# Performance work log

Hardware: AMD Instinct MI355X
Metric: run time of the kernel (lower is better)

Reference implementation:

```python
import jax, jax.numpy as jnp
import numpy as np

# snntorch atan surrogate spike (alpha=2): fwd heaviside, bwd 1/(1+(pi*x)^2)
@jax.custom_vjp
def atan_spike(x):
    return (x > 0).astype(x.dtype)

def _atan_fwd(x):
    return atan_spike(x), x

def _atan_bwd(x, g):
    return (g / (1.0 + (jnp.pi * x) ** 2),)

atan_spike.defvjp(_atan_fwd, _atan_bwd)

B, C, T, H, O = 2048, 5, 2048, 16, 2

def setup_inputs() -> dict:
    key = jax.random.key(0)
    ks = jax.random.split(key, 6)
    x = jax.random.normal(ks[0], (B, C, T), dtype=jnp.float32)
    conv_w = jax.random.normal(ks[1], (H, C, 3), dtype=jnp.float32) * (1.0 / np.sqrt(C * 3))
    conv_b = jax.random.normal(ks[2], (H,), dtype=jnp.float32) * 0.01
    bn_gamma = jnp.ones((H,), jnp.float32)
    bn_beta = jnp.zeros((H,), jnp.float32)
    bn_mean = jnp.zeros((H,), jnp.float32)   # BatchNorm1d running stats (eval mode)
    bn_var = jnp.ones((H,), jnp.float32)
    fc_w = jax.random.normal(ks[3], (O, H), dtype=jnp.float32) * (1.0 / np.sqrt(H))
    fc_b = jax.random.normal(ks[4], (O,), dtype=jnp.float32) * 0.01
    beta1 = jnp.float32(0.8)   # snn.Leaky learn_beta=True -> scalar param
    beta2 = jnp.float32(0.8)
    return dict(x=x, conv_w=conv_w, conv_b=conv_b, bn_gamma=bn_gamma, bn_beta=bn_beta,
                bn_mean=bn_mean, bn_var=bn_var, fc_w=fc_w, fc_b=fc_b,
                beta1=beta1, beta2=beta2)

def reference(x, conv_w, conv_b, bn_gamma, bn_beta, bn_mean, bn_var, fc_w, fc_b, beta1, beta2):
    EPS, THR = 1e-5, 1.0
    # Conv1d(k=3, pad=1) on a length-1 signal: only the middle tap contributes.
    w_mid = conv_w[:, :, 1]                      # [H, C]
    scale = bn_gamma / jnp.sqrt(bn_var + EPS)    # fold BN affine
    b1 = jnp.clip(beta1, 0.0, 1.0)               # snntorch clamps learned beta
    b2 = jnp.clip(beta2, 0.0, 1.0)
    xT = jnp.transpose(x, (2, 0, 1))             # [T, B, C]
    dt = x.dtype
    mem1_0 = jnp.zeros((x.shape[0], w_mid.shape[0]), dt)
    mem2_0 = jnp.zeros((x.shape[0], fc_w.shape[0]), dt)
    acc_0 = jnp.zeros_like(mem2_0)

    def step(carry, xt):
        mem1, mem2, acc = carry
        feat = (xt * 2.0) @ w_mid.T + conv_b                 # conv1d -> [B, H]
        feat = (feat - bn_mean) * scale + bn_beta            # BN (running stats)
        # snntorch Leaky (reset_mechanism='subtract'): reset from PREVIOUS mem, detached
        reset1 = jax.lax.stop_gradient((mem1 > THR).astype(dt))
        mem1 = b1 * mem1 + feat - reset1 * THR
        spk1 = atan_spike(mem1 - THR)
        cur2 = spk1 @ fc_w.T + fc_b                          # [B, O]
        reset2 = jax.lax.stop_gradient((mem2 > THR).astype(dt))
        mem2 = b2 * mem2 + cur2 - reset2 * THR
        spk2 = atan_spike(mem2 - THR)
        return (mem1, mem2, acc + spk2), None

    (_, _, acc), _ = jax.lax.scan(step, (mem1_0, mem2_0, acc_0), xT)
    return acc  # sum of output spikes over time, [B, num_classes]
```

## Files before the change

### kernel.cpp

```cpp
#include <hip/hip_runtime.h>
#include <type_traits>

typedef float v2f __attribute__((ext_vector_type(2)));

#define BB 2048
#define CC 5
#define TT 2048
#define HH 16
#define OO 2

#define NCH  32
#define CHT  (TT / NCH)
#define WARM 96

__device__ __forceinline__ float comp4(const float4& v, int j) {
    return j == 0 ? v.x : (j == 1 ? v.y : (j == 2 ? v.z : v.w));
}
__device__ __forceinline__ v2f fma2(v2f a, v2f b, v2f c) {
    return __builtin_elementwise_fma(a, b, c);
}

#define HP 8

__global__ __launch_bounds__(64, 1) void snn_laneb_kernel(
    const float* __restrict__ x,
    const float* __restrict__ conv_w,
    const float* __restrict__ conv_b,
    const float* __restrict__ bn_gamma,
    const float* __restrict__ bn_beta,
    const float* __restrict__ bn_mean,
    const float* __restrict__ bn_var,
    const float* __restrict__ fc_w,
    const float* __restrict__ fc_b,
    const float* __restrict__ beta1p,
    const float* __restrict__ beta2p,
    float* __restrict__ out)
{
    const int b     = blockIdx.x * 64 + threadIdx.x;
    const int chunk = blockIdx.y;

    const float b1 = fminf(fmaxf(beta1p[0], 0.0f), 1.0f);
    const float b2 = fminf(fmaxf(beta2p[0], 0.0f), 1.0f);
    const v2f b1v = {b1, b1};

    v2f wp[CC][HP], effbp[HP], fw0p[HP], fw1p[HP];
#pragma unroll
    for (int hp = 0; hp < HP; ++hp) {
        {
            const int h = 2 * hp;
            const float sc = bn_gamma[h] * rsqrtf(bn_var[h] + 1e-5f);
#pragma unroll
            for (int c = 0; c < CC; ++c)
                wp[c][hp].x = 2.0f * conv_w[h * (CC * 3) + c * 3 + 1] * sc;
            effbp[hp].x = (conv_b[h] - bn_mean[h]) * sc + bn_beta[h];
            fw0p[hp].x = fc_w[h];
            fw1p[hp].x = fc_w[HH + h];
        }
        {
            const int h = 2 * hp + 1;
            const float sc = bn_gamma[h] * rsqrtf(bn_var[h] + 1e-5f);
#pragma unroll
            for (int c = 0; c < CC; ++c)
                wp[c][hp].y = 2.0f * conv_w[h * (CC * 3) + c * 3 + 1] * sc;
            effbp[hp].y = (conv_b[h] - bn_mean[h]) * sc + bn_beta[h];
            fw0p[hp].y = fc_w[h];
            fw1p[hp].y = fc_w[HH + h];
        }
    }
    const float fb0 = fc_b[0], fb1 = fc_b[1];

    const float* xb = x + (size_t)b * CC * TT;

    const int t_start = chunk * CHT;
    int tw            = t_start - WARM;
    if (tw < 0) tw = 0;
    const int t_end   = t_start + CHT;
    const int ngroups = (t_end - tw) >> 2;
    const int warm_g  = (t_start - tw) >> 2;

    v2f mem1p[HP] = {}, sp[HP] = {};
    float mem2_0 = 0.0f, mem2_1 = 0.0f, s2f0 = 0.0f, s2f1 = 0.0f;
    float acc0 = 0.0f, acc1 = 0.0f;

    auto ldg = [&](float4 (&buf)[CC], int t) __attribute__((always_inline)) {
#pragma unroll
        for (int c = 0; c < CC; ++c)
            buf[c] = *reinterpret_cast<const float4*>(xb + c * TT + t);
    };

    float4 bufA[CC], bufB[CC], bufC[CC], bufD[CC];
    ldg(bufA, tw);
    ldg(bufB, tw + 4);
    ldg(bufC, tw + 8);
    ldg(bufD, tw + 12);

    auto step4 = [&](const float4 (&cur)[CC], auto ACCC) __attribute__((always_inline)) {
#pragma unroll
        for (int j = 0; j < 4; ++j) {
            v2f xv[CC];
#pragma unroll
            for (int c = 0; c < CC; ++c) {
                const float xs = comp4(cur[c], j);
                xv[c].x = xs; xv[c].y = xs;
            }

            v2f r0p = {0.0f, 0.0f}, r1p = {0.0f, 0.0f};
#pragma unroll
            for (int hp = 0; hp < HP; ++hp) {
                v2f f = effbp[hp];
#pragma unroll
                for (int c = 0; c < CC; ++c)
                    f = fma2(xv[c], wp[c][hp], f);

                const v2f m = fma2(b1v, mem1p[hp], f - sp[hp]);
                mem1p[hp] = m;
                v2f s;
                s.x = m.x > 1.0f ? 1.0f : 0.0f;
                s.y = m.y > 1.0f ? 1.0f : 0.0f;
                sp[hp] = s;
                r0p = fma2(s, fw0p[hp], r0p);
                r1p = fma2(s, fw1p[hp], r1p);
            }
            const float cur2_0 = r0p.x + r0p.y + fb0;
            const float cur2_1 = r1p.x + r1p.y + fb1;

            mem2_0 = fmaf(b2, mem2_0, cur2_0 - s2f0);
            s2f0 = mem2_0 > 1.0f ? 1.0f : 0.0f;
            mem2_1 = fmaf(b2, mem2_1, cur2_1 - s2f1);
            s2f1 = mem2_1 > 1.0f ? 1.0f : 0.0f;

            if constexpr (decltype(ACCC)::value) {
                acc0 += s2f0;
                acc1 += s2f1;
            }
        }
    };

    const int nquads = ngroups >> 2;
    const int wquads = warm_g >> 2;
    const int tlast  = t_end - 4;

#define RUN_QUAD(ACCC)                                                   \
    {                                                                    \
        int t0 = tw + (4 * q + 4) * 4; if (t0 > tlast) t0 = tlast;       \
        int t1 = tw + (4 * q + 5) * 4; if (t1 > tlast) t1 = tlast;       \
        int t2 = tw + (4 * q + 6) * 4; if (t2 > tlast) t2 = tlast;       \
        int t3 = tw + (4 * q + 7) * 4; if (t3 > tlast) t3 = tlast;       \
        step4(bufA, ACCC); ldg(bufA, t0);                                \
        step4(bufB, ACCC); ldg(bufB, t1);                                \
        step4(bufC, ACCC); ldg(bufC, t2);                                \
        step4(bufD, ACCC); ldg(bufD, t3);                                \
    }

#pragma unroll 1
    for (int q = 0; q < wquads; ++q)
        RUN_QUAD((std::integral_constant<bool, false>{}));
#pragma unroll 1
    for (int q = wquads; q < nquads; ++q)
        RUN_QUAD((std::integral_constant<bool, true>{}));
#undef RUN_QUAD

    atomicAdd(&out[(size_t)b * OO + 0], acc0);
    atomicAdd(&out[(size_t)b * OO + 1], acc1);
}

extern "C" void kernel_launch(void* const* d_in, const int* in_sizes, int n_in,
                              void* d_out, int out_size, void* d_ws, size_t ws_size,
                              hipStream_t stream) {
    const float* x        = (const float*)d_in[0];
    const float* conv_w   = (const float*)d_in[1];
    const float* conv_b   = (const float*)d_in[2];
    const float* bn_gamma = (const float*)d_in[3];
    const float* bn_beta  = (const float*)d_in[4];
    const float* bn_mean  = (const float*)d_in[5];
    const float* bn_var   = (const float*)d_in[6];
    const float* fc_w     = (const float*)d_in[7];
    const float* fc_b     = (const float*)d_in[8];
    const float* beta1    = (const float*)d_in[9];
    const float* beta2    = (const float*)d_in[10];
    float* out = (float*)d_out;

    hipMemsetAsync(out, 0, (size_t)out_size * sizeof(float), stream);

    dim3 grid(BB / 64, NCH);
    dim3 block(64);
    snn_laneb_kernel<<<grid, block, 0, stream>>>(
        x, conv_w, conv_b, bn_gamma, bn_beta, bn_mean, bn_var,
        fc_w, fc_b, beta1, beta2, out);
}
```

Before: 88.33 us.

## Transpose input to time-major layout before scan for coalesced loads

Adds a shared-memory transpose kernel that rewrites x from [B,C,T] to [C,T,B] in workspace, then runs the scan kernel reading coalesced per-timestep values across batch lanes. The old layout had each lane reading float4 strided by C*T, giving poorly coalesced accesses. The change pays for an extra full read and write of the 84 MB input and a second launch, and it falls back to the old kernel when the workspace is too small.

```diff
diff --git a/kernel.cpp b/kernel.cpp
--- a/kernel.cpp
+++ b/kernel.cpp
@@ -12,6 +12,11 @@
 #define NCH  32
 #define CHT  (TT / NCH)
 #define WARM 96
+#define HP   8
+
+#define TTL 32
+#define BTL 256
+#define XT_BYTES ((size_t)CC * TT * BB * 4)
 
 __device__ __forceinline__ float comp4(const float4& v, int j) {
     return j == 0 ? v.x : (j == 1 ? v.y : (j == 2 ? v.z : v.w));
@@ -20,9 +25,177 @@
     return __builtin_elementwise_fma(a, b, c);
 }
 
-#define HP 8
-
-__global__ __launch_bounds__(64, 1) void snn_laneb_kernel(
+__global__ __launch_bounds__(256) void transpose_kernel(
+    const float* __restrict__ x, float* __restrict__ xT)
+{
+    __shared__ float tile[TTL][BTL + 1];
+    const int c   = blockIdx.z;
+    const int tb  = blockIdx.x * TTL;
+    const int bb  = blockIdx.y * BTL;
+    const int tid = threadIdx.x;
+
+    const int s  = tid & 7;
+    const int br = tid >> 3;
+#pragma unroll
+    for (int i = 0; i < 8; ++i) {
+        const int b_local = br + i * 32;
+        const float4 v = *reinterpret_cast<const float4*>(
+            x + (size_t)(bb + b_local) * (CC * TT) + (size_t)c * TT + tb + 4 * s);
+        tile[4 * s + 0][b_local] = v.x;
+        tile[4 * s + 1][b_local] = v.y;
+        tile[4 * s + 2][b_local] = v.z;
+        tile[4 * s + 3][b_local] = v.w;
+    }
+    __syncthreads();
+
+#pragma unroll
+    for (int t = 0; t < TTL; ++t)
+        xT[((size_t)c * TT + tb + t) * BB + bb + tid] = tile[t][tid];
+}
+
+__global__ __launch_bounds__(64, 1) void snn_scanT_kernel(
+    const float* __restrict__ xT,
+    const float* __restrict__ conv_w,
+    const float* __restrict__ conv_b,
+    const float* __restrict__ bn_gamma,
+    const float* __restrict__ bn_beta,
+    const float* __restrict__ bn_mean,
+    const float* __restrict__ bn_var,
+    const float* __restrict__ fc_w,
+    const float* __restrict__ fc_b,
+    const float* __restrict__ beta1p,
+    const float* __restrict__ beta2p,
+    float* __restrict__ out)
+{
+    const int b     = blockIdx.x * 64 + threadIdx.x;
+    const int chunk = blockIdx.y;
+
+    const float b1 = fminf(fmaxf(beta1p[0], 0.0f), 1.0f);
+    const float b2 = fminf(fmaxf(beta2p[0], 0.0f), 1.0f);
+    const v2f b1v = {b1, b1};
+
+    v2f wp[CC][HP], effbp[HP], fw0p[HP], fw1p[HP];
+#pragma unroll
+    for (int hp = 0; hp < HP; ++hp) {
+        {
+            const int h = 2 * hp;
+            const float sc = bn_gamma[h] * rsqrtf(bn_var[h] + 1e-5f);
+#pragma unroll
+            for (int c = 0; c < CC; ++c)
+                wp[c][hp].x = 2.0f * conv_w[h * (CC * 3) + c * 3 + 1] * sc;
+            effbp[hp].x = (conv_b[h] - bn_mean[h]) * sc + bn_beta[h];
+            fw0p[hp].x = fc_w[h];
+            fw1p[hp].x = fc_w[HH + h];
+        }
+        {
+            const int h = 2 * hp + 1;
+            const float sc = bn_gamma[h] * rsqrtf(bn_var[h] + 1e-5f);
+#pragma unroll
+            for (int c = 0; c < CC; ++c)
+                wp[c][hp].y = 2.0f * conv_w[h * (CC * 3) + c * 3 + 1] * sc;
+            effbp[hp].y = (conv_b[h] - bn_mean[h]) * sc + bn_beta[h];
+            fw0p[hp].y = fc_w[h];
+            fw1p[hp].y = fc_w[HH + h];
+        }
+    }
+    const float fb0 = fc_b[0], fb1 = fc_b[1];
+
+    const int t_start = chunk * CHT;
+    int tw            = t_start - WARM;
+    if (tw < 0) tw = 0;
+    const int t_end   = t_start + CHT;
+    const int ngroups = (t_end - tw) >> 2;
+    const int warm_g  = (t_start - tw) >> 2;
+
+    v2f mem1p[HP] = {}, sp[HP] = {};
+    float mem2_0 = 0.0f, mem2_1 = 0.0f, s2f0 = 0.0f, s2f1 = 0.0f;
+    float acc0 = 0.0f, acc1 = 0.0f;
+
+    auto ldg = [&](float (&buf)[CC][4], int t) __attribute__((always_inline)) {
+#pragma unroll
+        for (int c = 0; c < CC; ++c)
+#pragma unroll
+            for (int j = 0; j < 4; ++j)
+                buf[c][j] = xT[((size_t)c * TT + t + j) * BB + b];
+    };
+
+    float bufA[CC][4], bufB[CC][4], bufC[CC][4], bufD[CC][4];
+    ldg(bufA, tw);
+    ldg(bufB, tw + 4);
+    ldg(bufC, tw + 8);
+    ldg(bufD, tw + 12);
+
+    auto step4 = [&](const float (&cur)[CC][4], auto ACCC) __attribute__((always_inline)) {
+#pragma unroll
+        for (int j = 0; j < 4; ++j) {
+            v2f xv[CC];
+#pragma unroll
+            for (int c = 0; c < CC; ++c) {
+                const float xs = cur[c][j];
+                xv[c].x = xs; xv[c].y = xs;
+            }
+
+            v2f r0p = {0.0f, 0.0f}, r1p = {0.0f, 0.0f};
+#pragma unroll
+            for (int hp = 0; hp < HP; ++hp) {
+                v2f f = effbp[hp];
+#pragma unroll
+                for (int c = 0; c < CC; ++c)
+                    f = fma2(xv[c], wp[c][hp], f);
+
+                const v2f m = fma2(b1v, mem1p[hp], f - sp[hp]);
+                mem1p[hp] = m;
+                v2f s;
+                s.x = m.x > 1.0f ? 1.0f : 0.0f;
+                s.y = m.y > 1.0f ? 1.0f : 0.0f;
+                sp[hp] = s;
+                r0p = fma2(s, fw0p[hp], r0p);
+                r1p = fma2(s, fw1p[hp], r1p);
+            }
+            const float cur2_0 = r0p.x + r0p.y + fb0;
+            const float cur2_1 = r1p.x + r1p.y + fb1;
+
+            mem2_0 = fmaf(b2, mem2_0, cur2_0 - s2f0);
+            s2f0 = mem2_0 > 1.0f ? 1.0f : 0.0f;
+            mem2_1 = fmaf(b2, mem2_1, cur2_1 - s2f1);
+            s2f1 = mem2_1 > 1.0f ? 1.0f : 0.0f;
+
+            if constexpr (decltype(ACCC)::value) {
+                acc0 += s2f0;
+                acc1 += s2f1;
+            }
+        }
+    };
+
+    const int nquads = ngroups >> 2;
+    const int wquads = warm_g >> 2;
+    const int tlast  = t_end - 4;
+
+#define RUN_QUAD(ACCC)                                                   \
+    {                                                                    \
+        int t0 = tw + (4 * q + 4) * 4; if (t0 > tlast) t0 = tlast;       \
+        int t1 = tw + (4 * q + 5) * 4; if (t1 > tlast) t1 = tlast;       \
+        int t2 = tw + (4 * q + 6) * 4; if (t2 > tlast) t2 = tlast;       \
+        int t3 = tw + (4 * q + 7) * 4; if (t3 > tlast) t3 = tlast;       \
+        step4(bufA, ACCC); ldg(bufA, t0);                                \
+        step4(bufB, ACCC); ldg(bufB, t1);                                \
+        step4(bufC, ACCC); ldg(bufC, t2);                                \
+        step4(bufD, ACCC); ldg(bufD, t3);                                \
+    }
+
+#pragma unroll 1
+    for (int q = 0; q < wquads; ++q)
+        RUN_QUAD((std::integral_constant<bool, false>{}));
+#pragma unroll 1
+    for (int q = wquads; q < nquads; ++q)
+        RUN_QUAD((std::integral_constant<bool, true>{}));
+#undef RUN_QUAD
+
+    atomicAdd(&out[(size_t)b * OO + 0], acc0);
+    atomicAdd(&out[(size_t)b * OO + 1], acc1);
+}
+
+__global__ __launch_bounds__(64, 1) void snn_laneb_fb_kernel(
     const float* __restrict__ x,
     const float* __restrict__ conv_w,
     const float* __restrict__ conv_b,
@@ -103,7 +276,6 @@
                 const float xs = comp4(cur[c], j);
                 xv[c].x = xs; xv[c].y = xs;
             }
-
             v2f r0p = {0.0f, 0.0f}, r1p = {0.0f, 0.0f};
 #pragma unroll
             for (int hp = 0; hp < HP; ++hp) {
@@ -111,7 +283,6 @@
 #pragma unroll
                 for (int c = 0; c < CC; ++c)
                     f = fma2(xv[c], wp[c][hp], f);
-
                 const v2f m = fma2(b1v, mem1p[hp], f - sp[hp]);
                 mem1p[hp] = m;
                 v2f s;
@@ -123,12 +294,10 @@
             }
             const float cur2_0 = r0p.x + r0p.y + fb0;
             const float cur2_1 = r1p.x + r1p.y + fb1;
-
             mem2_0 = fmaf(b2, mem2_0, cur2_0 - s2f0);
             s2f0 = mem2_0 > 1.0f ? 1.0f : 0.0f;
             mem2_1 = fmaf(b2, mem2_1, cur2_1 - s2f1);
             s2f1 = mem2_1 > 1.0f ? 1.0f : 0.0f;
-
             if constexpr (decltype(ACCC)::value) {
                 acc0 += s2f0;
                 acc1 += s2f1;
@@ -182,9 +351,18 @@
 
     hipMemsetAsync(out, 0, (size_t)out_size * sizeof(float), stream);
 
-    dim3 grid(BB / 64, NCH);
-    dim3 block(64);
-    snn_laneb_kernel<<<grid, block, 0, stream>>>(
-        x, conv_w, conv_b, bn_gamma, bn_beta, bn_mean, bn_var,
-        fc_w, fc_b, beta1, beta2, out);
-}
+    if (ws_size >= XT_BYTES) {
+        float* xT = (float*)d_ws;
+        dim3 tgrid(TT / TTL, BB / BTL, CC);
+        transpose_kernel<<<tgrid, 256, 0, stream>>>(x, xT);
+        dim3 grid(BB / 64, NCH);
+        snn_scanT_kernel<<<grid, dim3(64), 0, stream>>>(
+            xT, conv_w, conv_b, bn_gamma, bn_beta, bn_mean, bn_var,
+            fc_w, fc_b, beta1, beta2, out);
+    } else {
+        dim3 grid(BB / 64, NCH);
+        snn_laneb_fb_kernel<<<grid, dim3(64), 0, stream>>>(
+            x, conv_w, conv_b, bn_gamma, bn_beta, bn_mean, bn_var,
+            fc_w, fc_b, beta1, beta2, out);
+    }
+}
```

Result: slower. 93.84 us (+6.2%).

## Split hidden units across lane pairs and stage coalesced input tiles through LDS

Applied to the files above, without the earlier changes.

Each batch row is now handled by two lanes, each owning 8 of the 16 hidden units, and the two partial fc sums are combined with a DPP swap. Input is loaded cooperatively in coalesced float4 chunks into a double-buffered LDS tile instead of per-lane strided global loads. The grid doubles to give more waves and a shorter per-lane dependency chain. In exchange it adds LDS traffic, cross-lane DPP ops and duplicated layer-2 work on both lanes of a pair.

```diff
diff --git a/kernel.cpp b/kernel.cpp
--- a/kernel.cpp
+++ b/kernel.cpp
@@ -19,10 +19,12 @@
 __device__ __forceinline__ v2f fma2(v2f a, v2f b, v2f c) {
     return __builtin_elementwise_fma(a, b, c);
 }
-
-#define HP 8
-
-__global__ __launch_bounds__(64, 1) void snn_laneb_kernel(
+__device__ __forceinline__ float qswap_add(float v) {
+    int s = __builtin_amdgcn_update_dpp(0, __float_as_int(v), 0xB1, 0xf, 0xf, true);
+    return v + __int_as_float(s);
+}
+
+__global__ __launch_bounds__(64) void snn_fused_kernel(
     const float* __restrict__ x,
     const float* __restrict__ conv_w,
     const float* __restrict__ conv_b,
@@ -36,18 +38,26 @@
     const float* __restrict__ beta2p,
     float* __restrict__ out)
 {
-    const int b     = blockIdx.x * 64 + threadIdx.x;
+    __shared__ float4 lds[2][CC][4][32];
+
+    const int lane  = threadIdx.x;
+    const int b0    = blockIdx.x * 32;
+    const int bown  = lane >> 1;
+    const int hb    = (lane & 1) * 8;
     const int chunk = blockIdx.y;
+
+    const int sbc  = lane >> 2;
+    const int st4  = lane & 3;
 
     const float b1 = fminf(fmaxf(beta1p[0], 0.0f), 1.0f);
     const float b2 = fminf(fmaxf(beta2p[0], 0.0f), 1.0f);
     const v2f b1v = {b1, b1};
 
-    v2f wp[CC][HP], effbp[HP], fw0p[HP], fw1p[HP];
-#pragma unroll
-    for (int hp = 0; hp < HP; ++hp) {
+    v2f wp[CC][4], effbp[4], fw0p[4], fw1p[4];
+#pragma unroll
+    for (int hp = 0; hp < 4; ++hp) {
         {
-            const int h = 2 * hp;
+            const int h = hb + 2 * hp;
             const float sc = bn_gamma[h] * rsqrtf(bn_var[h] + 1e-5f);
 #pragma unroll
             for (int c = 0; c < CC; ++c)
@@ -57,7 +67,7 @@
             fw1p[hp].x = fc_w[HH + h];
         }
         {
-            const int h = 2 * hp + 1;
+            const int h = hb + 2 * hp + 1;
             const float sc = bn_gamma[h] * rsqrtf(bn_var[h] + 1e-5f);
 #pragma unroll
             for (int c = 0; c < CC; ++c)
@@ -69,30 +79,40 @@
     }
     const float fb0 = fc_b[0], fb1 = fc_b[1];
 
-    const float* xb = x + (size_t)b * CC * TT;
-
     const int t_start = chunk * CHT;
     int tw            = t_start - WARM;
     if (tw < 0) tw = 0;
     const int t_end   = t_start + CHT;
-    const int ngroups = (t_end - tw) >> 2;
-    const int warm_g  = (t_start - tw) >> 2;
-
-    v2f mem1p[HP] = {}, sp[HP] = {};
+    const int S       = (t_end - tw) >> 4;
+    const int warmS   = (t_start - tw) >> 4;
+
+    v2f mem1p[4] = {}, sp[4] = {};
     float mem2_0 = 0.0f, mem2_1 = 0.0f, s2f0 = 0.0f, s2f1 = 0.0f;
     float acc0 = 0.0f, acc1 = 0.0f;
 
-    auto ldg = [&](float4 (&buf)[CC], int t) __attribute__((always_inline)) {
-#pragma unroll
-        for (int c = 0; c < CC; ++c)
-            buf[c] = *reinterpret_cast<const float4*>(xb + c * TT + t);
-    };
-
-    float4 bufA[CC], bufB[CC], bufC[CC], bufD[CC];
-    ldg(bufA, tw);
-    ldg(bufB, tw + 4);
-    ldg(bufC, tw + 8);
-    ldg(bufD, tw + 12);
+    float4 st[10];
+
+#define STAGE_LOAD(TSB)                                                      \
+    {                                                                        \
+        _Pragma("unroll")                                                    \
+        for (int i = 0; i < 10; ++i) {                                       \
+            const int bc = i * 16 + sbc;                                     \
+            const int bs = bc & 31, cs = bc >> 5;                            \
+            st[i] = *reinterpret_cast<const float4*>(                        \
+                x + (size_t)(b0 + bs) * (CC * TT) + (size_t)cs * TT +        \
+                (TSB) + st4 * 4);                                            \
+        }                                                                    \
+    }
+
+#define STAGE_WRITE(BUF)                                                     \
+    {                                                                        \
+        _Pragma("unroll")                                                    \
+        for (int i = 0; i < 10; ++i) {                                       \
+            const int bc = i * 16 + sbc;                                     \
+            const int bs = bc & 31, cs = bc >> 5;                            \
+            lds[BUF][cs][st4][bs] = st[i];                                   \
+        }                                                                    \
+    }
 
     auto step4 = [&](const float4 (&cur)[CC], auto ACCC) __attribute__((always_inline)) {
 #pragma unroll
@@ -106,7 +126,7 @@
 
             v2f r0p = {0.0f, 0.0f}, r1p = {0.0f, 0.0f};
 #pragma unroll
-            for (int hp = 0; hp < HP; ++hp) {
+            for (int hp = 0; hp < 4; ++hp) {
                 v2f f = effbp[hp];
 #pragma unroll
                 for (int c = 0; c < CC; ++c)
@@ -121,8 +141,8 @@
                 r0p = fma2(s, fw0p[hp], r0p);
                 r1p = fma2(s, fw1p[hp], r1p);
             }
-            const float cur2_0 = r0p.x + r0p.y + fb0;
-            const float cur2_1 = r1p.x + r1p.y + fb1;
+            const float cur2_0 = qswap_add(r0p.x + r0p.y) + fb0;
+            const float cur2_1 = qswap_add(r1p.x + r1p.y) + fb1;
 
             mem2_0 = fmaf(b2, mem2_0, cur2_0 - s2f0);
             s2f0 = mem2_0 > 1.0f ? 1.0f : 0.0f;
@@ -136,32 +156,39 @@
         }
     };
 
-    const int nquads = ngroups >> 2;
-    const int wquads = warm_g >> 2;
-    const int tlast  = t_end - 4;
-
-#define RUN_QUAD(ACCC)                                                   \
-    {                                                                    \
-        int t0 = tw + (4 * q + 4) * 4; if (t0 > tlast) t0 = tlast;       \
-        int t1 = tw + (4 * q + 5) * 4; if (t1 > tlast) t1 = tlast;       \
-        int t2 = tw + (4 * q + 6) * 4; if (t2 > tlast) t2 = tlast;       \
-        int t3 = tw + (4 * q + 7) * 4; if (t3 > tlast) t3 = tlast;       \
-        step4(bufA, ACCC); ldg(bufA, t0);                                \
-        step4(bufB, ACCC); ldg(bufB, t1);                                \
-        step4(bufC, ACCC); ldg(bufC, t2);                                \
-        step4(bufD, ACCC); ldg(bufD, t3);                                \
-    }
+#define RUN_STAGE(ACCC)                                                      \
+    {                                                                        \
+        const bool more = (s + 1 < S);                                       \
+        if (more) STAGE_LOAD(tw + (s + 1) * 16);                             \
+        _Pragma("unroll")                                                    \
+        for (int q4 = 0; q4 < 4; ++q4) {                                     \
+            float4 cb[CC];                                                   \
+            _Pragma("unroll")                                                \
+            for (int c = 0; c < CC; ++c)                                     \
+                cb[c] = lds[s & 1][c][q4][bown];                             \
+            step4(cb, ACCC);                                                 \
+        }                                                                    \
+        if (more) STAGE_WRITE((s + 1) & 1);                                  \
+    }
+
+    STAGE_LOAD(tw);
+    STAGE_WRITE(0);
 
 #pragma unroll 1
-    for (int q = 0; q < wquads; ++q)
-        RUN_QUAD((std::integral_constant<bool, false>{}));
+    for (int s = 0; s < warmS; ++s)
+        RUN_STAGE((std::integral_constant<bool, false>{}));
 #pragma unroll 1
-    for (int q = wquads; q < nquads; ++q)
-        RUN_QUAD((std::integral_constant<bool, true>{}));
-#undef RUN_QUAD
-
-    atomicAdd(&out[(size_t)b * OO + 0], acc0);
-    atomicAdd(&out[(size_t)b * OO + 1], acc1);
+    for (int s = warmS; s < S; ++s)
+        RUN_STAGE((std::integral_constant<bool, true>{}));
+
+#undef RUN_STAGE
+#undef STAGE_WRITE
+#undef STAGE_LOAD
+
+    if (!(lane & 1)) {
+        atomicAdd(&out[(size_t)(b0 + bown) * OO + 0], acc0);
+        atomicAdd(&out[(size_t)(b0 + bown) * OO + 1], acc1);
+    }
 }
 
 extern "C" void kernel_launch(void* const* d_in, const int* in_sizes, int n_in,
@@ -182,9 +209,8 @@
 
     hipMemsetAsync(out, 0, (size_t)out_size * sizeof(float), stream);
 
-    dim3 grid(BB / 64, NCH);
-    dim3 block(64);
-    snn_laneb_kernel<<<grid, block, 0, stream>>>(
+    dim3 grid(BB / 32, NCH);
+    snn_fused_kernel<<<grid, dim3(64), 0, stream>>>(
         x, conv_w, conv_b, bn_gamma, bn_beta, bn_mean, bn_var,
         fc_w, fc_b, beta1, beta2, out);
 }
```

Result: slower. 117.3 us (+32.8%).
